# Optimization experiments

Measured on AMD Instinct MI355X. Metric: run time of the kernel, lower is better.

## Reference

```python
import jax, jax.numpy as jnp
import numpy as np
from jax.scipy.linalg import solve_triangular

B = 131072; OBS = 128; AD = 8; H = 64; FH = 32; NL = 4
D1 = AD // 2; D2 = AD - D1; TRIL = AD * (AD + 1) // 2
_rows, _cols = np.tril_indices(AD)          # same row-major order as torch.tril_indices
_diag = (_rows == _cols)                    # bool mask over TRIL entries
_diag_pos = np.where(_diag)[0]
LOG2PI = float(np.log(2.0 * np.pi))
EPS = float(np.finfo(np.float32).eps)       # torch RMSNorm default eps = finfo.eps


def _rms(x, w):
    return x * jax.lax.rsqrt(jnp.mean(x * x, axis=-1, keepdims=True) + EPS) * w


def setup_inputs() -> dict:
    ks = iter(jax.random.split(jax.random.key(0), 32))
    def w(shape, scale):
        return jax.random.normal(next(ks), shape, jnp.float32) * scale
    z = lambda *s: jnp.zeros(s, jnp.float32)
    return dict(
        x=jax.random.normal(next(ks), (B, OBS), jnp.float32),
        action=jax.random.normal(next(ks), (B, AD), jnp.float32),
        z_rpo=jax.random.uniform(next(ks), (B, AD), jnp.float32, -0.1, 0.1),
        cW1=w((OBS, H), OBS ** -0.5), cb1=z(H), c_rms=jnp.ones(H, jnp.float32),
        cW2=w((H, H), H ** -0.5), cb2=z(H), cW3=w((H, 1), H ** -0.5), cb3=z(1),
        aW1=w((OBS, H), OBS ** -0.5), ab1=z(H), aW2=w((H, H), H ** -0.5), ab2=z(H),
        mW=w((H, AD), 0.01), mb=z(AD),
        tW1=w((OBS, H), OBS ** -0.5), tb1=z(H), t_rms1=jnp.ones(H, jnp.float32),
        tW2=w((H, H), H ** -0.5), tb2=z(H), t_rms2=jnp.ones(H, jnp.float32),
        hW=w((H, TRIL), 0.01), hb=z(TRIL),
        fW1=w((NL, D1 + OBS, FH), (D1 + OBS) ** -0.5), fb1=z(NL, FH),
        fW2=w((NL, FH, 2 * D2), 0.01), fb2=z(NL, 2 * D2),
    )


def reference(x, action, z_rpo, cW1, cb1, c_rms, cW2, cb2, cW3, cb3,
              aW1, ab1, aW2, ab2, mW, mb,
              tW1, tb1, t_rms1, tW2, tb2, t_rms2, hW, hb,
              fW1, fb1, fW2, fb2):
    silu = jax.nn.silu
    Bn = x.shape[0]
    # actor mean trunk + head, with RPO uniform perturbation (action is given)
    h = silu(silu(x @ aW1 + ab1) @ aW2 + ab2)
    action_mean = h @ mW + mb + z_rpo
    # state-dependent lower-triangular covariance factor
    tl = _rms(silu(x @ tW1 + tb1), t_rms1)
    tl = _rms(silu(tl @ tW2 + tb2), t_rms2)
    raw = tl @ hW + hb                                   # [B, TRIL]
    proc = jnp.where(_diag, jax.nn.softplus(raw), raw)
    L = jnp.zeros((Bn, AD, AD), raw.dtype).at[:, _rows, _cols].set(proc)
    log_det_L = jnp.log(proc[:, _diag_pos]).sum(-1)      # [B]
    # coupling flow inverse: noise -> correlated
    noise = action - action_mean
    x1, x2 = noise[:, :D1], noise[:, D1:]
    fld = jnp.zeros((Bn,), raw.dtype)
    for i in reversed(range(NL)):
        cond, y = (x1, x2) if i % 2 == 0 else (x2, x1)
        st = silu(jnp.concatenate([cond, x], -1) @ fW1[i] + fb1[i]) @ fW2[i] + fb2[i]
        s_raw, tshift = jnp.split(st, 2, -1)
        s = jnp.tanh(s_raw) * 2.0
        xt = (y - tshift) * jnp.exp(-s)
        if i % 2 == 0:
            x2 = xt
        else:
            x1 = xt
        fld = fld + s.sum(-1)
    correlated = jnp.concatenate([x1, x2], -1)           # [B, AD]
    zc = solve_triangular(L, correlated[..., None], lower=True)[..., 0]
    mahal = (zc * zc).sum(-1)
    log_prob = -0.5 * (AD * LOG2PI + mahal) - log_det_L - fld
    entropy = 0.5 * (AD * (1.0 + LOG2PI)) + log_det_L + fld
    # critic
    v = _rms(silu(x @ cW1 + cb1), c_rms)
    v = silu(v @ cW2 + cb2) @ cW3 + cb3                  # [B, 1]
    return (action, log_prob, entropy, v)
```

## Files before the change

kernel.cpp:

```cpp
#include <hip/hip_runtime.h>

typedef __attribute__((ext_vector_type(8))) short    v8s;
typedef __attribute__((ext_vector_type(4))) float    f4;
typedef __attribute__((ext_vector_type(2))) float    f2;
typedef __attribute__((ext_vector_type(2))) unsigned u32x2;

#define MFMA16 __builtin_amdgcn_mfma_f32_16x16x32_bf16

#define AW1T 0
#define TW1T 8192
#define CW1T 16384
#define AW2T 24576
#define TW2T 28672
#define CW2T 32768
#define MWT  36864
#define HWT  37888
#define FW1XT 40960
#define FW2T  57344
#define WS_BF16_TOTAL 59392
#define W1CTO 0
#define HBPO  512

#define LOG2PI 1.83787706640934548356f
#define EPSF   1.1920928955078125e-07f

__device__ __constant__ int PERM[36] = {0,2,5,9,14,20,27,35,
  1,3,4,6,7,8,10,11,12,13,15,16,17,18,19,21,22,23,24,25,26,28,29,30,31,32,33,34};

__device__ __forceinline__ float ubits(unsigned u){union{unsigned u;float f;}c;c.u=u;return c.f;}
__device__ __forceinline__ unsigned fbits(float f){union{float f;unsigned u;}c;c.f=f;return c.u;}
__device__ __forceinline__ float siluf(float v){ return v/(1.f+__expf(-v)); }
__device__ __forceinline__ unsigned pk2(float a,float b){
  unsigned ua=fbits(a); ua+=0x7fffu+((ua>>16)&1u);
  unsigned ub=fbits(b); ub+=0x7fffu+((ub>>16)&1u);
  return (ua>>16)|(ub&0xffff0000u);
}
__device__ __forceinline__ unsigned short f2bu(float a){
  unsigned ua=fbits(a); ua+=0x7fffu+((ua>>16)&1u);
  return (unsigned short)(ua>>16);
}
__device__ __forceinline__ float qsum(float v){
  v += __shfl_xor(v,16,64); v += __shfl_xor(v,32,64); return v;
}

__global__ __launch_bounds__(256)
void prep_kernel(const float* __restrict__ aW1, const float* __restrict__ aW2,
                 const float* __restrict__ mW,  const float* __restrict__ tW1,
                 const float* __restrict__ tW2, const float* __restrict__ hW,
                 const float* __restrict__ hb,  const float* __restrict__ cW1,
                 const float* __restrict__ cW2, const float* __restrict__ fW1,
                 const float* __restrict__ fW2,
                 unsigned short* __restrict__ ws16, float* __restrict__ wsf)
{
  const int tid = blockIdx.x*256 + threadIdx.x;
  const int stride = gridDim.x*256;
  for (int idx=tid; idx<64*128; idx+=stride){
    int n=idx>>7, k=idx&127;
    ws16[AW1T+idx]=f2bu(aW1[k*64+n]);
    ws16[TW1T+idx]=f2bu(tW1[k*64+n]);
    ws16[CW1T+idx]=f2bu(cW1[k*64+n]);
  }
  for (int idx=tid; idx<64*64; idx+=stride){
    int n=idx>>6, k=idx&63;
    ws16[AW2T+idx]=f2bu(aW2[k*64+n]);
    ws16[TW2T+idx]=f2bu(tW2[k*64+n]);
    ws16[CW2T+idx]=f2bu(cW2[k*64+n]);
  }
  for (int idx=tid; idx<16*64; idx+=stride){
    int n=idx>>6, k=idx&63;
    ws16[MWT+idx]=f2bu(n<8 ? mW[k*8+n] : 0.f);
  }
  for (int idx=tid; idx<48*64; idx+=stride){
    int n=idx>>6, k=idx&63;
    ws16[HWT+idx]=f2bu(n<36 ? hW[k*36+PERM[n]] : 0.f);
  }
  for (int idx=tid; idx<4*32*128; idx+=stride){
    int i=idx>>12, rem=idx&4095, n=rem>>7, k=rem&127;
    ws16[FW1XT+idx]=f2bu(fW1[i*4224 + (4+k)*32 + n]);
  }
  for (int idx=tid; idx<4*16*32; idx+=stride){
    int i=idx>>9, rem=idx&511, n=rem>>5, k=rem&31;
    ws16[FW2T+idx]=f2bu(n<8 ? fW2[i*256 + k*8 + n] : 0.f);
  }
  for (int idx=tid; idx<4*32*4; idx+=stride){
    int i=idx>>7, rem=idx&127, n=rem>>2, k=rem&3;
    wsf[W1CTO+idx]=fW1[i*4224 + k*32 + n];
  }
  for (int idx=tid; idx<48; idx+=stride)
    wsf[HBPO+idx] = idx<36 ? hb[PERM[idx]] : 0.f;
}

template<int NWT>
__device__ __forceinline__ void gemmX(const unsigned short* __restrict__ Wt,
                                      const v8s* __restrict__ xf,
                                      f4 (*acc)[4], int c, int q)
{
#pragma unroll
  for (int kt=0; kt<4; ++kt){
    v8s wf[NWT];
#pragma unroll
    for (int wt=0; wt<NWT; ++wt)
      wf[wt] = *(const v8s*)(Wt + (wt*16 + c)*128 + kt*32 + q*8);
#pragma unroll
    for (int wt=0; wt<NWT; ++wt)
#pragma unroll
      for (int et=0; et<4; ++et)
        acc[wt][et] = MFMA16(wf[wt], xf[et*4+kt], acc[wt][et], 0,0,0);
  }
}

template<int NWT>
__device__ __forceinline__ void gemmH(const unsigned short* __restrict__ Wt,
                                      const unsigned short* __restrict__ actL,
                                      f4 (*acc)[4], int c, int q)
{
#pragma unroll
  for (int kt=0; kt<2; ++kt){
    v8s wf[NWT];
#pragma unroll
    for (int wt=0; wt<NWT; ++wt)
      wf[wt] = *(const v8s*)(Wt + (wt*16 + c)*64 + kt*32 + q*8);
    v8s af[4];
#pragma unroll
    for (int et=0; et<4; ++et)
      af[et] = *(const v8s*)(actL + (et*16+c)*72 + kt*32 + q*8);
#pragma unroll
    for (int wt=0; wt<NWT; ++wt)
#pragma unroll
      for (int et=0; et<4; ++et)
        acc[wt][et] = MFMA16(wf[wt], af[et], acc[wt][et], 0,0,0);
  }
}

__global__ __launch_bounds__(64,2)
void policy_kernel(
    const float* __restrict__ x,    const float* __restrict__ action, const float* __restrict__ z_rpo,
    const float* __restrict__ cb1,  const float* __restrict__ c_rms,  const float* __restrict__ cb2,
    const float* __restrict__ cW3,  const float* __restrict__ cb3,
    const float* __restrict__ ab1,  const float* __restrict__ ab2,    const float* __restrict__ mb,
    const float* __restrict__ tb1,  const float* __restrict__ t_rms1, const float* __restrict__ tb2,
    const float* __restrict__ t_rms2,
    const float* __restrict__ fb1,  const float* __restrict__ fb2,
    const unsigned short* __restrict__ ws16, const float* __restrict__ wsf,
    float* __restrict__ out, const int Btot)
{
  const int lane = threadIdx.x;
  const int q = lane >> 4, c = lane & 15;
  const int b0 = blockIdx.x << 6;

  __shared__ alignas(16) unsigned char smem[19968];
  unsigned short* actL = (unsigned short*)smem;
  unsigned short* hidL = (unsigned short*)smem;
  unsigned short* triL = (unsigned short*)(smem + 9216);
  float*          nstL = (float*)(smem + 14848);
  float*          amL  = (float*)(smem + 17408);

  v8s xf[16];
  {
    const float* xb = x + (size_t)b0*128;
#pragma unroll
    for (int et=0; et<4; ++et)
#pragma unroll
      for (int kt=0; kt<4; ++kt){
        const float* p = xb + (size_t)(et*16+c)*128 + kt*32 + q*8;
        f4 u0 = *(const f4*)p, u1 = *(const f4*)(p+4);
        union { unsigned u[4]; v8s v; } r;
        r.u[0]=pk2(u0[0],u0[1]); r.u[1]=pk2(u0[2],u0[3]);
        r.u[2]=pk2(u1[0],u1[1]); r.u[3]=pk2(u1[2],u1[3]);
        xf[et*4+kt] = r.v;
      }
  }

  f4 acc[4][4];
  const f4 z4 = {0.f,0.f,0.f,0.f};

#pragma unroll
  for (int wt=0; wt<4; ++wt) for (int et=0; et<4; ++et) acc[wt][et]=z4;
  gemmX<4>(ws16+AW1T, xf, acc, c, q);
#pragma unroll
  for (int wt=0; wt<4; ++wt){
    const f4 bv = *(const f4*)(ab1 + wt*16 + q*4);
#pragma unroll
    for (int et=0; et<4; ++et){
      float s0=siluf(acc[wt][et][0]+bv[0]), s1=siluf(acc[wt][et][1]+bv[1]);
      float s2=siluf(acc[wt][et][2]+bv[2]), s3=siluf(acc[wt][et][3]+bv[3]);
      u32x2 u = {pk2(s0,s1), pk2(s2,s3)};
      *(u32x2*)(actL + (et*16+c)*72 + wt*16 + q*4) = u;
    }
  }
#pragma unroll
  for (int wt=0; wt<4; ++wt) for (int et=0; et<4; ++et) acc[wt][et]=z4;
  gemmH<4>(ws16+AW2T, actL, acc, c, q);
#pragma unroll
  for (int wt=0; wt<4; ++wt){
    const f4 bv = *(const f4*)(ab2 + wt*16 + q*4);
#pragma unroll
    for (int et=0; et<4; ++et){
      float s0=siluf(acc[wt][et][0]+bv[0]), s1=siluf(acc[wt][et][1]+bv[1]);
      float s2=siluf(acc[wt][et][2]+bv[2]), s3=siluf(acc[wt][et][3]+bv[3]);
      u32x2 u = {pk2(s0,s1), pk2(s2,s3)};
      *(u32x2*)(actL + (et*16+c)*72 + wt*16 + q*4) = u;
    }
  }
  {
    f4 am1[1][4]; am1[0][0]=z4; am1[0][1]=z4; am1[0][2]=z4; am1[0][3]=z4;
    gemmH<1>(ws16+MWT, actL, am1, c, q);
    if (q<2){
      const f4 mbv = *(const f4*)(mb + q*4);
#pragma unroll
      for (int et=0; et<4; ++et){
        float* p = amL + (et*16+c)*10 + q*4;
        *(f2*)p     = (f2){am1[0][et][0]+mbv[0], am1[0][et][1]+mbv[1]};
        *(f2*)(p+2) = (f2){am1[0][et][2]+mbv[2], am1[0][et][3]+mbv[3]};
      }
    }
  }

#pragma unroll
  for (int wt=0; wt<4; ++wt) for (int et=0; et<4; ++et) acc[wt][et]=z4;
  gemmX<4>(ws16+TW1T, xf, acc, c, q);
  float r1[4];
  {
    float ss[4]={0.f,0.f,0.f,0.f};
#pragma unroll
    for (int wt=0; wt<4; ++wt){
      const f4 bv = *(const f4*)(tb1 + wt*16 + q*4);
      const f4 rw = *(const f4*)(t_rms1 + wt*16 + q*4);
#pragma unroll
      for (int et=0; et<4; ++et){
        float s0=siluf(acc[wt][et][0]+bv[0]), s1=siluf(acc[wt][et][1]+bv[1]);
        float s2=siluf(acc[wt][et][2]+bv[2]), s3=siluf(acc[wt][et][3]+bv[3]);
        ss[et] += s0*s0+s1*s1+s2*s2+s3*s3;
        u32x2 u = {pk2(s0*rw[0],s1*rw[1]), pk2(s2*rw[2],s3*rw[3])};
        *(u32x2*)(actL + (et*16+c)*72 + wt*16 + q*4) = u;
      }
    }
#pragma unroll
    for (int et=0; et<4; ++et) r1[et]=rsqrtf(qsum(ss[et])*(1.f/64.f)+EPSF);
  }
#pragma unroll
  for (int wt=0; wt<4; ++wt) for (int et=0; et<4; ++et) acc[wt][et]=z4;
  gemmH<4>(ws16+TW2T, actL, acc, c, q);
  float r2[4];
  {
    float ss[4]={0.f,0.f,0.f,0.f};
#pragma unroll
    for (int wt=0; wt<4; ++wt){
      const f4 bv = *(const f4*)(tb2 + wt*16 + q*4);
      const f4 rw = *(const f4*)(t_rms2 + wt*16 + q*4);
#pragma unroll
      for (int et=0; et<4; ++et){
        float s0=siluf(r1[et]*acc[wt][et][0]+bv[0]), s1=siluf(r1[et]*acc[wt][et][1]+bv[1]);
        float s2=siluf(r1[et]*acc[wt][et][2]+bv[2]), s3=siluf(r1[et]*acc[wt][et][3]+bv[3]);
        ss[et] += s0*s0+s1*s1+s2*s2+s3*s3;
        u32x2 u = {pk2(s0*rw[0],s1*rw[1]), pk2(s2*rw[2],s3*rw[3])};
        *(u32x2*)(actL + (et*16+c)*72 + wt*16 + q*4) = u;
      }
    }
#pragma unroll
    for (int et=0; et<4; ++et) r2[et]=rsqrtf(qsum(ss[et])*(1.f/64.f)+EPSF);
  }
  float ldet[4];
  {
    f4 a3[3][4];
#pragma unroll
    for (int wt=0; wt<3; ++wt) for (int et=0; et<4; ++et) a3[wt][et]=z4;
    gemmH<3>(ws16+HWT, actL, a3, c, q);
    float ldp[4]={0.f,0.f,0.f,0.f};
#pragma unroll
    for (int wt=0; wt<3; ++wt){
      const f4 hbv = *(const f4*)(wsf + HBPO + wt*16 + q*4);
#pragma unroll
      for (int et=0; et<4; ++et){
        float t0=r2[et]*a3[wt][et][0]+hbv[0], t1=r2[et]*a3[wt][et][1]+hbv[1];
        float t2=r2[et]*a3[wt][et][2]+hbv[2], t3=r2[et]*a3[wt][et][3]+hbv[3];
        if (wt==0 && q<2){
          t0=fmaxf(t0,0.f)+__logf(1.f+__expf(-fabsf(t0)));
          t1=fmaxf(t1,0.f)+__logf(1.f+__expf(-fabsf(t1)));
          t2=fmaxf(t2,0.f)+__logf(1.f+__expf(-fabsf(t2)));
          t3=fmaxf(t3,0.f)+__logf(1.f+__expf(-fabsf(t3)));
          ldp[et] += __logf(t0)+__logf(t1)+__logf(t2)+__logf(t3);
        }
        if (wt<2 || q==0){
          u32x2 u = {pk2(t0,t1), pk2(t2,t3)};
          *(u32x2*)(triL + (et*16+c)*44 + wt*16 + q*4) = u;
        }
      }
    }
#pragma unroll
    for (int et=0; et<4; ++et) ldet[et]=qsum(ldp[et]);
  }

#pragma unroll
  for (int wt=0; wt<4; ++wt) for (int et=0; et<4; ++et) acc[wt][et]=z4;
  gemmX<4>(ws16+CW1T, xf, acc, c, q);
  float rc[4];
  {
    float ss[4]={0.f,0.f,0.f,0.f};
#pragma unroll
    for (int wt=0; wt<4; ++wt){
      const f4 bv = *(const f4*)(cb1 + wt*16 + q*4);
      const f4 rw = *(const f4*)(c_rms + wt*16 + q*4);
#pragma unroll
      for (int et=0; et<4; ++et){
        float s0=siluf(acc[wt][et][0]+bv[0]), s1=siluf(acc[wt][et][1]+bv[1]);
        float s2=siluf(acc[wt][et][2]+bv[2]), s3=siluf(acc[wt][et][3]+bv[3]);
        ss[et] += s0*s0+s1*s1+s2*s2+s3*s3;
        u32x2 u = {pk2(s0*rw[0],s1*rw[1]), pk2(s2*rw[2],s3*rw[3])};
        *(u32x2*)(actL + (et*16+c)*72 + wt*16 + q*4) = u;
      }
    }
#pragma unroll
    for (int et=0; et<4; ++et) rc[et]=rsqrtf(qsum(ss[et])*(1.f/64.f)+EPSF);
  }
  float vv[4];
  {
#pragma unroll
    for (int wt=0; wt<4; ++wt) for (int et=0; et<4; ++et) acc[wt][et]=z4;
    gemmH<4>(ws16+CW2T, actL, acc, c, q);
    float vp[4]={0.f,0.f,0.f,0.f};
#pragma unroll
    for (int wt=0; wt<4; ++wt){
      const f4 bv = *(const f4*)(cb2 + wt*16 + q*4);
      const f4 wv = *(const f4*)(cW3 + wt*16 + q*4);
#pragma unroll
      for (int et=0; et<4; ++et){
        vp[et] = fmaf(siluf(rc[et]*acc[wt][et][0]+bv[0]), wv[0], vp[et]);
        vp[et] = fmaf(siluf(rc[et]*acc[wt][et][1]+bv[1]), wv[1], vp[et]);
        vp[et] = fmaf(siluf(rc[et]*acc[wt][et][2]+bv[2]), wv[2], vp[et]);
        vp[et] = fmaf(siluf(rc[et]*acc[wt][et][3]+bv[3]), wv[3], vp[et]);
      }
    }
    const float cb3v = cb3[0];
#pragma unroll
    for (int et=0; et<4; ++et) vv[et]=qsum(vp[et])+cb3v;
  }

  const int l = lane;
  const size_t bb = (size_t)(b0+l)*8;
  float nst[8], fld=0.f;
  {
    f4 a0=*(const f4*)(action+bb), a1=*(const f4*)(action+bb+4);
    f4 zr0=*(const f4*)(z_rpo+bb), zr1=*(const f4*)(z_rpo+bb+4);
    *(f4*)(out+bb)=a0; *(f4*)(out+bb+4)=a1;
#pragma unroll
    for (int j=0;j<4;++j){
      nst[j]   = a0[j]-amL[l*10+j]  -zr0[j];
      nst[4+j] = a1[j]-amL[l*10+4+j]-zr1[j];
    }
#pragma unroll
    for (int j=0;j<8;++j) nstL[l*10+j]=nst[j];
  }

#pragma unroll
  for (int ii=0; ii<4; ++ii){
    const int i = 3-ii;
    const int cb = (i&1)?4:0, yb = (i&1)?0:4;
    f4 a2[2][4];
#pragma unroll
    for (int wt=0; wt<2; ++wt) for (int et=0; et<4; ++et) a2[wt][et]=z4;
    gemmX<2>(ws16+FW1XT+i*4096, xf, a2, c, q);
    float nv[4][4];
#pragma unroll
    for (int et=0; et<4; ++et){
      const float* np = nstL + (et*16+c)*10 + cb;
      f2 t0=*(const f2*)np, t1=*(const f2*)(np+2);
      nv[et][0]=t0[0]; nv[et][1]=t0[1]; nv[et][2]=t1[0]; nv[et][3]=t1[1];
    }
#pragma unroll
    for (int wt=0; wt<2; ++wt){
      const f4 bv = *(const f4*)(fb1 + i*32 + wt*16 + q*4);
      float sh[4][4];
#pragma unroll
      for (int r=0; r<4; ++r){
        const f4 wc = *(const f4*)(wsf + W1CTO + i*128 + (wt*16+q*4+r)*4);
#pragma unroll
        for (int et=0; et<4; ++et){
          float hv = a2[wt][et][r] + bv[r]
                   + wc[0]*nv[et][0] + wc[1]*nv[et][1]
                   + wc[2]*nv[et][2] + wc[3]*nv[et][3];
          sh[et][r] = siluf(hv);
        }
      }
#pragma unroll
      for (int et=0; et<4; ++et){
        u32x2 u = {pk2(sh[et][0],sh[et][1]), pk2(sh[et][2],sh[et][3])};
        *(u32x2*)(hidL + (et*16+c)*40 + wt*16 + q*4) = u;
      }
    }
    {
      const v8s wf3 = *(const v8s*)(ws16 + FW2T + i*512 + c*32 + q*8);
      f4 as[4];
#pragma unroll
      for (int et=0; et<4; ++et){
        const v8s hf = *(const v8s*)(hidL + (et*16+c)*40 + q*8);
        f4 a1s = z4;
        a1s = MFMA16(wf3, hf, a1s, 0,0,0);
        as[et]=a1s;
      }
      if (q<2){
        const f4 fbv = *(const f4*)(fb2 + i*8 + q*4);
#pragma unroll
        for (int et=0; et<4; ++et){
          float* p = amL + (et*16+c)*10 + q*4;
          *(f2*)p     = (f2){as[et][0]+fbv[0], as[et][1]+fbv[1]};
          *(f2*)(p+2) = (f2){as[et][2]+fbv[2], as[et][3]+fbv[3]};
        }
      }
    }
    {
      float sr0=amL[l*10+0], sr1=amL[l*10+1], sr2=amL[l*10+2], sr3=amL[l*10+3];
      float th0=amL[l*10+4], th1=amL[l*10+5], th2=amL[l*10+6], th3=amL[l*10+7];
      float s0=2.f-4.f/(__expf(2.f*sr0)+1.f);
      float s1=2.f-4.f/(__expf(2.f*sr1)+1.f);
      float s2=2.f-4.f/(__expf(2.f*sr2)+1.f);
      float s3=2.f-4.f/(__expf(2.f*sr3)+1.f);
      nst[yb+0]=(nst[yb+0]-th0)*__expf(-s0);
      nst[yb+1]=(nst[yb+1]-th1)*__expf(-s1);
      nst[yb+2]=(nst[yb+2]-th2)*__expf(-s2);
      nst[yb+3]=(nst[yb+3]-th3)*__expf(-s3);
      nstL[l*10+yb+0]=nst[yb+0]; nstL[l*10+yb+1]=nst[yb+1];
      nstL[l*10+yb+2]=nst[yb+2]; nstL[l*10+yb+3]=nst[yb+3];
      fld += s0+s1+s2+s3;
    }
  }

  {
    constexpr int INVPERM[36] = {0,8,1,9,10,2,11,12,13,3,14,15,16,17,4,18,19,20,
                                 21,22,5,23,24,25,26,27,28,6,29,30,31,32,33,34,35,7};
    float tri[36];
#pragma unroll
    for (int j=0;j<36;++j){
      unsigned h = triL[l*44 + INVPERM[j]];
      tri[j] = ubits(h<<16);
    }
    float zv[8], mahal=0.f;
#pragma unroll
    for (int r=0;r<8;++r){
      float s=nst[r];
      const int base=(r*(r+1))>>1;
#pragma unroll
      for (int cc=0;cc<r;++cc) s -= tri[base+cc]*zv[cc];
      const float z = s/tri[base+r];
      zv[r]=z; mahal+=z*z;
    }
    const float ldet_s = (l<16)?ldet[0]:(l<32)?ldet[1]:(l<48)?ldet[2]:ldet[3];
    const float v_s    = (l<16)?vv[0]:(l<32)?vv[1]:(l<48)?vv[2]:vv[3];
    const float lp = -0.5f*(8.f*LOG2PI+mahal) - ldet_s - fld;
    const float en =  0.5f*(8.f*(1.f+LOG2PI)) + ldet_s + fld;
    out[(size_t)Btot*8  + b0 + l] = lp;
    out[(size_t)Btot*9  + b0 + l] = en;
    out[(size_t)Btot*10 + b0 + l] = v_s;
  }
}

extern "C" void kernel_launch(void* const* d_in, const int* in_sizes, int n_in,
                              void* d_out, int out_size, void* d_ws, size_t ws_size,
                              hipStream_t stream) {
  const float* x      = (const float*)d_in[0];
  const float* action = (const float*)d_in[1];
  const float* z_rpo  = (const float*)d_in[2];
  const float* cW1    = (const float*)d_in[3];
  const float* cb1    = (const float*)d_in[4];
  const float* c_rms  = (const float*)d_in[5];
  const float* cW2    = (const float*)d_in[6];
  const float* cb2    = (const float*)d_in[7];
  const float* cW3    = (const float*)d_in[8];
  const float* cb3    = (const float*)d_in[9];
  const float* aW1    = (const float*)d_in[10];
  const float* ab1    = (const float*)d_in[11];
  const float* aW2    = (const float*)d_in[12];
  const float* ab2    = (const float*)d_in[13];
  const float* mW     = (const float*)d_in[14];
  const float* mb     = (const float*)d_in[15];
  const float* tW1    = (const float*)d_in[16];
  const float* tb1    = (const float*)d_in[17];
  const float* t_rms1 = (const float*)d_in[18];
  const float* tW2    = (const float*)d_in[19];
  const float* tb2    = (const float*)d_in[20];
  const float* t_rms2 = (const float*)d_in[21];
  const float* hW     = (const float*)d_in[22];
  const float* hb     = (const float*)d_in[23];
  const float* fW1    = (const float*)d_in[24];
  const float* fb1    = (const float*)d_in[25];
  const float* fW2    = (const float*)d_in[26];
  const float* fb2    = (const float*)d_in[27];
  float* out = (float*)d_out;

  unsigned short* ws16 = (unsigned short*)d_ws;
  float* wsf = (float*)((char*)d_ws + WS_BF16_TOTAL*2);

  const int Btot = in_sizes[0] / 128;

  hipLaunchKernelGGL(prep_kernel, dim3(64), dim3(256), 0, stream,
                     aW1, aW2, mW, tW1, tW2, hW, hb, cW1, cW2, fW1, fW2, ws16, wsf);
  hipLaunchKernelGGL(policy_kernel, dim3(Btot/64), dim3(64), 0, stream,
                     x, action, z_rpo, cb1, c_rms, cb2, cW3, cb3,
                     ab1, ab2, mb, tb1, t_rms1, tb2, t_rms2, fb1, fb2,
                     ws16, wsf, out, Btot);
}
```

Before: 213.5 us.

## Swizzle LDS activations, shrink shared memory, raise occupancy, use fast reciprocals

Replaces the padded LDS activation layout with an XOR-swizzled 64-wide layout, shrinks the triangular and mean/flow buffers and stores the flow-head outputs as bf16, cutting LDS per block. Launch bounds change from 2 to 4 blocks per SIMD so more waves can overlap latency, which may force register spills given the large per-lane register arrays. Divisions in silu, tanh and the triangular solve become hardware rcp approximations, and the prep kernel grid doubles. Storing flow scale/shift in bf16 adds rounding error to the log-prob computation.

```diff
diff --git a/kernel.cpp b/kernel.cpp
--- a/kernel.cpp
+++ b/kernel.cpp
@@ -29,7 +29,8 @@
 
 __device__ __forceinline__ float ubits(unsigned u){union{unsigned u;float f;}c;c.u=u;return c.f;}
 __device__ __forceinline__ unsigned fbits(float f){union{float f;unsigned u;}c;c.f=f;return c.u;}
-__device__ __forceinline__ float siluf(float v){ return v/(1.f+__expf(-v)); }
+__device__ __forceinline__ float rcpf(float x){ return __builtin_amdgcn_rcpf(x); }
+__device__ __forceinline__ float siluf(float v){ return v * rcpf(1.f + __expf(-v)); }
 __device__ __forceinline__ unsigned pk2(float a,float b){
   unsigned ua=fbits(a); ua+=0x7fffu+((ua>>16)&1u);
   unsigned ub=fbits(b); ub+=0x7fffu+((ub>>16)&1u);
@@ -39,9 +40,11 @@
   unsigned ua=fbits(a); ua+=0x7fffu+((ua>>16)&1u);
   return (unsigned short)(ua>>16);
 }
+__device__ __forceinline__ float b2f16(unsigned short h){ return ubits(((unsigned)h)<<16); }
 __device__ __forceinline__ float qsum(float v){
   v += __shfl_xor(v,16,64); v += __shfl_xor(v,32,64); return v;
 }
+__device__ __forceinline__ int swz(int row, int blk){ return row*64 + ((blk ^ (row&7))*8); }
 
 __global__ __launch_bounds__(256)
 void prep_kernel(const float* __restrict__ aW1, const float* __restrict__ aW2,
@@ -123,7 +126,7 @@
     v8s af[4];
 #pragma unroll
     for (int et=0; et<4; ++et)
-      af[et] = *(const v8s*)(actL + (et*16+c)*72 + kt*32 + q*8);
+      af[et] = *(const v8s*)(actL + swz(et*16+c, kt*4+q));
 #pragma unroll
     for (int wt=0; wt<NWT; ++wt)
 #pragma unroll
@@ -132,7 +135,7 @@
   }
 }
 
-__global__ __launch_bounds__(64,2)
+__global__ __launch_bounds__(64,4)
 void policy_kernel(
     const float* __restrict__ x,    const float* __restrict__ action, const float* __restrict__ z_rpo,
     const float* __restrict__ cb1,  const float* __restrict__ c_rms,  const float* __restrict__ cb2,
@@ -148,12 +151,12 @@
   const int q = lane >> 4, c = lane & 15;
   const int b0 = blockIdx.x << 6;
 
-  __shared__ alignas(16) unsigned char smem[19968];
+  __shared__ alignas(16) unsigned char smem[15872];
   unsigned short* actL = (unsigned short*)smem;
   unsigned short* hidL = (unsigned short*)smem;
-  unsigned short* triL = (unsigned short*)(smem + 9216);
-  float*          nstL = (float*)(smem + 14848);
-  float*          amL  = (float*)(smem + 17408);
+  unsigned short* triL = (unsigned short*)(smem + 8192);
+  float*          nstL = (float*)(smem + 12800);
+  unsigned short* amL  = (unsigned short*)(smem + 14848);
 
   v8s xf[16];
   {
@@ -185,7 +188,7 @@
       float s0=siluf(acc[wt][et][0]+bv[0]), s1=siluf(acc[wt][et][1]+bv[1]);
       float s2=siluf(acc[wt][et][2]+bv[2]), s3=siluf(acc[wt][et][3]+bv[3]);
       u32x2 u = {pk2(s0,s1), pk2(s2,s3)};
-      *(u32x2*)(actL + (et*16+c)*72 + wt*16 + q*4) = u;
+      *(u32x2*)(actL + swz(et*16+c, wt*2+(q>>1)) + (q&1)*4) = u;
     }
   }
 #pragma unroll
@@ -199,7 +202,7 @@
       float s0=siluf(acc[wt][et][0]+bv[0]), s1=siluf(acc[wt][et][1]+bv[1]);
       float s2=siluf(acc[wt][et][2]+bv[2]), s3=siluf(acc[wt][et][3]+bv[3]);
       u32x2 u = {pk2(s0,s1), pk2(s2,s3)};
-      *(u32x2*)(actL + (et*16+c)*72 + wt*16 + q*4) = u;
+      *(u32x2*)(actL + swz(et*16+c, wt*2+(q>>1)) + (q&1)*4) = u;
     }
   }
   {
@@ -209,9 +212,9 @@
       const f4 mbv = *(const f4*)(mb + q*4);
 #pragma unroll
       for (int et=0; et<4; ++et){
-        float* p = amL + (et*16+c)*10 + q*4;
-        *(f2*)p     = (f2){am1[0][et][0]+mbv[0], am1[0][et][1]+mbv[1]};
-        *(f2*)(p+2) = (f2){am1[0][et][2]+mbv[2], am1[0][et][3]+mbv[3]};
+        u32x2 u = {pk2(am1[0][et][0]+mbv[0], am1[0][et][1]+mbv[1]),
+                   pk2(am1[0][et][2]+mbv[2], am1[0][et][3]+mbv[3])};
+        *(u32x2*)(amL + (et*16+c)*8 + q*4) = u;
       }
     }
   }
@@ -232,7 +235,7 @@
         float s2=siluf(acc[wt][et][2]+bv[2]), s3=siluf(acc[wt][et][3]+bv[3]);
         ss[et] += s0*s0+s1*s1+s2*s2+s3*s3;
         u32x2 u = {pk2(s0*rw[0],s1*rw[1]), pk2(s2*rw[2],s3*rw[3])};
-        *(u32x2*)(actL + (et*16+c)*72 + wt*16 + q*4) = u;
+        *(u32x2*)(actL + swz(et*16+c, wt*2+(q>>1)) + (q&1)*4) = u;
       }
     }
 #pragma unroll
@@ -254,7 +257,7 @@
         float s2=siluf(r1[et]*acc[wt][et][2]+bv[2]), s3=siluf(r1[et]*acc[wt][et][3]+bv[3]);
         ss[et] += s0*s0+s1*s1+s2*s2+s3*s3;
         u32x2 u = {pk2(s0*rw[0],s1*rw[1]), pk2(s2*rw[2],s3*rw[3])};
-        *(u32x2*)(actL + (et*16+c)*72 + wt*16 + q*4) = u;
+        *(u32x2*)(actL + swz(et*16+c, wt*2+(q>>1)) + (q&1)*4) = u;
       }
     }
 #pragma unroll
@@ -283,7 +286,7 @@
         }
         if (wt<2 || q==0){
           u32x2 u = {pk2(t0,t1), pk2(t2,t3)};
-          *(u32x2*)(triL + (et*16+c)*44 + wt*16 + q*4) = u;
+          *(u32x2*)(triL + (et*16+c)*36 + wt*16 + q*4) = u;
         }
       }
     }
@@ -307,7 +310,7 @@
         float s2=siluf(acc[wt][et][2]+bv[2]), s3=siluf(acc[wt][et][3]+bv[3]);
         ss[et] += s0*s0+s1*s1+s2*s2+s3*s3;
         u32x2 u = {pk2(s0*rw[0],s1*rw[1]), pk2(s2*rw[2],s3*rw[3])};
-        *(u32x2*)(actL + (et*16+c)*72 + wt*16 + q*4) = u;
+        *(u32x2*)(actL + swz(et*16+c, wt*2+(q>>1)) + (q&1)*4) = u;
       }
     }
 #pragma unroll
@@ -345,11 +348,11 @@
     *(f4*)(out+bb)=a0; *(f4*)(out+bb+4)=a1;
 #pragma unroll
     for (int j=0;j<4;++j){
-      nst[j]   = a0[j]-amL[l*10+j]  -zr0[j];
-      nst[4+j] = a1[j]-amL[l*10+4+j]-zr1[j];
-    }
-#pragma unroll
-    for (int j=0;j<8;++j) nstL[l*10+j]=nst[j];
+      nst[j]   = a0[j]-b2f16(amL[l*8+j])  -zr0[j];
+      nst[4+j] = a1[j]-b2f16(amL[l*8+4+j])-zr1[j];
+    }
+    *(f4*)(nstL + l*8)     = (f4){nst[0],nst[1],nst[2],nst[3]};
+    *(f4*)(nstL + l*8 + 4) = (f4){nst[4],nst[5],nst[6],nst[7]};
   }
 
 #pragma unroll
@@ -363,7 +366,7 @@
     float nv[4][4];
 #pragma unroll
     for (int et=0; et<4; ++et){
-      const float* np = nstL + (et*16+c)*10 + cb;
+      const float* np = nstL + (et*16+c)*8 + cb;
       f2 t0=*(const f2*)np, t1=*(const f2*)(np+2);
       nv[et][0]=t0[0]; nv[et][1]=t0[1]; nv[et][2]=t1[0]; nv[et][3]=t1[1];
     }
@@ -385,7 +388,7 @@
 #pragma unroll
       for (int et=0; et<4; ++et){
         u32x2 u = {pk2(sh[et][0],sh[et][1]), pk2(sh[et][2],sh[et][3])};
-        *(u32x2*)(hidL + (et*16+c)*40 + wt*16 + q*4) = u;
+        *(u32x2*)(hidL + swz(et*16+c, wt*2+(q>>1)) + (q&1)*4) = u;
       }
     }
     {
@@ -393,7 +396,7 @@
       f4 as[4];
 #pragma unroll
       for (int et=0; et<4; ++et){
-        const v8s hf = *(const v8s*)(hidL + (et*16+c)*40 + q*8);
+        const v8s hf = *(const v8s*)(hidL + swz(et*16+c, q));
         f4 a1s = z4;
         a1s = MFMA16(wf3, hf, a1s, 0,0,0);
         as[et]=a1s;
@@ -402,25 +405,26 @@
         const f4 fbv = *(const f4*)(fb2 + i*8 + q*4);
 #pragma unroll
         for (int et=0; et<4; ++et){
-          float* p = amL + (et*16+c)*10 + q*4;
-          *(f2*)p     = (f2){as[et][0]+fbv[0], as[et][1]+fbv[1]};
-          *(f2*)(p+2) = (f2){as[et][2]+fbv[2], as[et][3]+fbv[3]};
+          u32x2 u = {pk2(as[et][0]+fbv[0], as[et][1]+fbv[1]),
+                     pk2(as[et][2]+fbv[2], as[et][3]+fbv[3])};
+          *(u32x2*)(amL + (et*16+c)*8 + q*4) = u;
         }
       }
     }
     {
-      float sr0=amL[l*10+0], sr1=amL[l*10+1], sr2=amL[l*10+2], sr3=amL[l*10+3];
-      float th0=amL[l*10+4], th1=amL[l*10+5], th2=amL[l*10+6], th3=amL[l*10+7];
-      float s0=2.f-4.f/(__expf(2.f*sr0)+1.f);
-      float s1=2.f-4.f/(__expf(2.f*sr1)+1.f);
-      float s2=2.f-4.f/(__expf(2.f*sr2)+1.f);
-      float s3=2.f-4.f/(__expf(2.f*sr3)+1.f);
+      float sr0=b2f16(amL[l*8+0]), sr1=b2f16(amL[l*8+1]);
+      float sr2=b2f16(amL[l*8+2]), sr3=b2f16(amL[l*8+3]);
+      float th0=b2f16(amL[l*8+4]), th1=b2f16(amL[l*8+5]);
+      float th2=b2f16(amL[l*8+6]), th3=b2f16(amL[l*8+7]);
+      float s0=2.f-4.f*rcpf(__expf(2.f*sr0)+1.f);
+      float s1=2.f-4.f*rcpf(__expf(2.f*sr1)+1.f);
+      float s2=2.f-4.f*rcpf(__expf(2.f*sr2)+1.f);
+      float s3=2.f-4.f*rcpf(__expf(2.f*sr3)+1.f);
       nst[yb+0]=(nst[yb+0]-th0)*__expf(-s0);
       nst[yb+1]=(nst[yb+1]-th1)*__expf(-s1);
       nst[yb+2]=(nst[yb+2]-th2)*__expf(-s2);
       nst[yb+3]=(nst[yb+3]-th3)*__expf(-s3);
-      nstL[l*10+yb+0]=nst[yb+0]; nstL[l*10+yb+1]=nst[yb+1];
-      nstL[l*10+yb+2]=nst[yb+2]; nstL[l*10+yb+3]=nst[yb+3];
+      *(f4*)(nstL + l*8 + yb) = (f4){nst[yb+0],nst[yb+1],nst[yb+2],nst[yb+3]};
       fld += s0+s1+s2+s3;
     }
   }
@@ -430,10 +434,7 @@
                                  21,22,5,23,24,25,26,27,28,6,29,30,31,32,33,34,35,7};
     float tri[36];
 #pragma unroll
-    for (int j=0;j<36;++j){
-      unsigned h = triL[l*44 + INVPERM[j]];
-      tri[j] = ubits(h<<16);
-    }
+    for (int j=0;j<36;++j) tri[j] = b2f16(triL[l*36 + INVPERM[j]]);
     float zv[8], mahal=0.f;
 #pragma unroll
     for (int r=0;r<8;++r){
@@ -441,7 +442,7 @@
       const int base=(r*(r+1))>>1;
 #pragma unroll
       for (int cc=0;cc<r;++cc) s -= tri[base+cc]*zv[cc];
-      const float z = s/tri[base+r];
+      const float z = s*rcpf(tri[base+r]);
       zv[r]=z; mahal+=z*z;
     }
     const float ldet_s = (l<16)?ldet[0]:(l<32)?ldet[1]:(l<48)?ldet[2]:ldet[3];
@@ -492,7 +493,7 @@
 
   const int Btot = in_sizes[0] / 128;
 
-  hipLaunchKernelGGL(prep_kernel, dim3(64), dim3(256), 0, stream,
+  hipLaunchKernelGGL(prep_kernel, dim3(128), dim3(256), 0, stream,
                      aW1, aW2, mW, tW1, tW2, hW, hb, cW1, cW2, fW1, fW2, ws16, wsf);
   hipLaunchKernelGGL(policy_kernel, dim3(Btot/64), dim3(64), 0, stream,
                      x, action, z_rpo, cb1, c_rms, cb2, cW3, cb3,
```

Result: no change. 212.7 us (-0.4%).
